# Performance work log

Hardware: AMD Instinct MI355X
Metric: run time of the kernel (lower is better)

Reference implementation:

```python
import jax, jax.numpy as jnp
import numpy as np
from jax import lax

NPOINT = 2048

def setup_inputs() -> dict:
    key = jax.random.key(0)
    B, C, N = 8, 3, 131072
    xyz = jax.random.normal(key, (B, C, N), dtype=jnp.float32)
    return {"xyz": xyz}

def reference(xyz) -> jnp.ndarray:
    # xyz: [B, 3, N] -> points [B, N, 3], as in the torch permute(0,2,1)
    pts = jnp.transpose(xyz, (0, 2, 1)).astype(jnp.float32)  # [B, N, 3]
    B, N, _ = pts.shape
    binds = jnp.arange(B)

    # PointNet++ furthest point sampling: first sampled index is 0,
    # maintain per-point min squared distance to the sampled set,
    # pick argmax each iteration.
    init_dist = jnp.full((B, N), 1e10, dtype=jnp.float32)
    init_idx = jnp.zeros((B,), dtype=jnp.int32)

    def step(carry, _):
        dist, last_idx = carry
        last = pts[binds, last_idx]                     # [B, 3]
        d = jnp.sum((pts - last[:, None, :]) ** 2, -1)  # [B, N]
        dist = jnp.minimum(dist, d)
        nxt = jnp.argmax(dist, axis=-1).astype(jnp.int32)
        return (dist, nxt), last_idx

    _, idxs = lax.scan(step, (init_dist, init_idx), None, length=NPOINT)
    return jnp.transpose(idxs, (1, 0))  # [B, npoint] int32 indices
```

## Files before the change

kernel.cpp:

```cpp
#include <hip/hip_runtime.h>
#include <stdint.h>


#define NB 8
#define NPTS 131072
#define NPOINT 2048
#define KBLK 32
#define BLOCK 512
#define PPT 8
#define NWAVES (BLOCK / 64)
#define PSTRIDE 8

__device__ uint64_t g_part[NB][KBLK * PSTRIDE];

static __device__ __forceinline__ uint64_t ld_rlx(uint64_t* p) {
  return __hip_atomic_load(p, __ATOMIC_RELAXED, __HIP_MEMORY_SCOPE_AGENT);
}
static __device__ __forceinline__ void st_rlx(uint64_t* p, uint64_t v) {
  __hip_atomic_store(p, v, __ATOMIC_RELAXED, __HIP_MEMORY_SCOPE_AGENT);
}

__global__ __launch_bounds__(BLOCK, 1) void fps_kernel(
    const float* __restrict__ xyz, int* __restrict__ out) {
  const int b = blockIdx.x & (NB - 1);
  const int k = blockIdx.x >> 3;
  const int tid = threadIdx.x;
  const int lane = tid & 63;
  const int wid = tid >> 6;

  const float* __restrict__ X = xyz + (size_t)b * 3u * NPTS;
  const float* __restrict__ Y = X + NPTS;
  const float* __restrict__ Z = Y + NPTS;

  const int base = k * (BLOCK * PPT);

  float px[PPT], py[PPT], pz[PPT], dist[PPT];
#pragma unroll
  for (int j = 0; j < PPT; ++j) {
    int i = base + j * BLOCK + tid;
    px[j] = X[i];
    py[j] = Y[i];
    pz[j] = Z[i];
    dist[j] = 1e10f;
  }

  __shared__ uint64_t sh_w[NWAVES];
  __shared__ int sh_idx;

  if (k == 0 && tid == 0) out[b * NPOINT] = 0;

  int cur = 0;

  for (int r = 1; r < NPOINT; ++r) {
    const int lu = __builtin_amdgcn_readfirstlane(cur);
    const float qx = X[lu];
    const float qy = Y[lu];
    const float qz = Z[lu];

    uint64_t pm = 0;
#pragma unroll
    for (int j = 0; j < PPT; ++j) {
      float dx = __fsub_rn(px[j], qx);
      float dy = __fsub_rn(py[j], qy);
      float dz = __fsub_rn(pz[j], qz);
      float d = __fadd_rn(__fadd_rn(__fmul_rn(dx, dx), __fmul_rn(dy, dy)),
                          __fmul_rn(dz, dz));
      float nd = fminf(dist[j], d);
      dist[j] = nd;
      uint32_t idx = (uint32_t)(base + j * BLOCK + tid);
      uint64_t cand = ((uint64_t)__float_as_uint(nd) << 32) |
                      ((uint64_t)(NPTS - 1u - idx) << 12);
      pm = cand > pm ? cand : pm;
    }

#pragma unroll
    for (int off = 32; off; off >>= 1) {
      uint64_t o = (uint64_t)__shfl_xor((unsigned long long)pm, off, 64);
      pm = o > pm ? o : pm;
    }
    if (lane == 0) sh_w[wid] = pm;
    __syncthreads();

    if (tid < 64) {
      uint64_t bm = (lane < NWAVES) ? sh_w[lane] : 0;
#pragma unroll
      for (int off = 4; off; off >>= 1) {
        uint64_t o = (uint64_t)__shfl_xor((unsigned long long)bm, off, 64);
        bm = o > bm ? o : bm;
      }
      if (tid == 0) st_rlx(&g_part[b][k * PSTRIDE], bm | (uint64_t)(uint32_t)r);

      uint64_t w = 0;
      if (lane < KBLK) {
        uint64_t* pp = &g_part[b][lane * PSTRIDE];
        do {
          w = ld_rlx(pp);
        } while ((w & 0xFFFull) != (uint64_t)(uint32_t)r);
      }
#pragma unroll
      for (int off = 16; off; off >>= 1) {
        uint64_t o = (uint64_t)__shfl_xor((unsigned long long)w, off, 64);
        w = o > w ? o : w;
      }
      if (tid == 0) {
        int widx = (int)(NPTS - 1u - (uint32_t)((w >> 12) & 0x1FFFFu));
        if (k == 0) out[b * NPOINT + r] = widx;
        sh_idx = widx;
      }
    }
    __syncthreads();
    cur = sh_idx;
  }
}

extern "C" void kernel_launch(void* const* d_in, const int* in_sizes, int n_in,
                              void* d_out, int out_size, void* d_ws,
                              size_t ws_size, hipStream_t stream) {
  (void)in_sizes; (void)n_in; (void)d_ws; (void)ws_size; (void)out_size;
  const float* xyz = (const float*)d_in[0];
  int* out = (int*)d_out;
  fps_kernel<<<dim3(NB * KBLK), dim3(BLOCK), 0, stream>>>(xyz, out);
}
```

Measured before the change: 4.581 ms.

## Replace block barriers with per-wave global slots and wave-level polling

Drops both __syncthreads per iteration. Each wave now publishes its own tagged partial max to a global slot (256 per batch), and every wave independently polls all slots and reduces them itself. This removes intra-block barrier latency and the single-wave serialization step. In exchange it adds global polling traffic from 8x more waves and denser slots with no padding, which may cause cache-line contention.

Measured after the change: 16.49 ms. 260% more time.

```diff
diff --git a/kernel.cpp b/kernel.cpp
--- a/kernel.cpp
+++ b/kernel.cpp
@@ -8,16 +8,21 @@
 #define KBLK 32
 #define BLOCK 512
 #define PPT 8
-#define NWAVES (BLOCK / 64)
-#define PSTRIDE 8
+#define WPB (BLOCK / 64)
+#define NSLOT (KBLK * WPB)
+#define SPL (NSLOT / 64)
 
-__device__ uint64_t g_part[NB][KBLK * PSTRIDE];
+__device__ uint64_t g_part[NB][NSLOT];
 
 static __device__ __forceinline__ uint64_t ld_rlx(uint64_t* p) {
   return __hip_atomic_load(p, __ATOMIC_RELAXED, __HIP_MEMORY_SCOPE_AGENT);
 }
 static __device__ __forceinline__ void st_rlx(uint64_t* p, uint64_t v) {
   __hip_atomic_store(p, v, __ATOMIC_RELAXED, __HIP_MEMORY_SCOPE_AGENT);
+}
+
+static __device__ __forceinline__ uint64_t max64(uint64_t a, uint64_t b) {
+  return a > b ? a : b;
 }
 
 __global__ __launch_bounds__(BLOCK, 1) void fps_kernel(
@@ -27,6 +32,7 @@
   const int tid = threadIdx.x;
   const int lane = tid & 63;
   const int wid = tid >> 6;
+  const int slot = k * WPB + wid;
 
   const float* __restrict__ X = xyz + (size_t)b * 3u * NPTS;
   const float* __restrict__ Y = X + NPTS;
@@ -43,9 +49,6 @@
     pz[j] = Z[i];
     dist[j] = 1e10f;
   }
-
-  __shared__ uint64_t sh_w[NWAVES];
-  __shared__ int sh_idx;
 
   if (k == 0 && tid == 0) out[b * NPOINT] = 0;
 
@@ -70,46 +73,40 @@
       uint32_t idx = (uint32_t)(base + j * BLOCK + tid);
       uint64_t cand = ((uint64_t)__float_as_uint(nd) << 32) |
                       ((uint64_t)(NPTS - 1u - idx) << 12);
-      pm = cand > pm ? cand : pm;
+      pm = max64(pm, cand);
     }
 
 #pragma unroll
     for (int off = 32; off; off >>= 1) {
       uint64_t o = (uint64_t)__shfl_xor((unsigned long long)pm, off, 64);
-      pm = o > pm ? o : pm;
+      pm = max64(pm, o);
     }
-    if (lane == 0) sh_w[wid] = pm;
-    __syncthreads();
 
-    if (tid < 64) {
-      uint64_t bm = (lane < NWAVES) ? sh_w[lane] : 0;
+    if (lane == 0) st_rlx(&g_part[b][slot], pm | (uint64_t)(uint32_t)r);
+
+    uint64_t* gp = &g_part[b][0];
+    uint64_t w0, w1, w2, w3;
+    const uint32_t tag = (uint32_t)r;
+    for (;;) {
+      w0 = ld_rlx(gp + lane);
+      w1 = ld_rlx(gp + lane + 64);
+      w2 = ld_rlx(gp + lane + 128);
+      w3 = ld_rlx(gp + lane + 192);
+      uint64_t bad = ((w0 ^ tag) | (w1 ^ tag) | (w2 ^ tag) | (w3 ^ tag)) &
+                     0xFFFull;
+      if (bad == 0) break;
+    }
+
+    uint64_t m = max64(max64(w0, w1), max64(w2, w3));
 #pragma unroll
-      for (int off = 4; off; off >>= 1) {
-        uint64_t o = (uint64_t)__shfl_xor((unsigned long long)bm, off, 64);
-        bm = o > bm ? o : bm;
-      }
-      if (tid == 0) st_rlx(&g_part[b][k * PSTRIDE], bm | (uint64_t)(uint32_t)r);
+    for (int off = 32; off; off >>= 1) {
+      uint64_t o = (uint64_t)__shfl_xor((unsigned long long)m, off, 64);
+      m = max64(m, o);
+    }
 
-      uint64_t w = 0;
-      if (lane < KBLK) {
-        uint64_t* pp = &g_part[b][lane * PSTRIDE];
-        do {
-          w = ld_rlx(pp);
-        } while ((w & 0xFFFull) != (uint64_t)(uint32_t)r);
-      }
-#pragma unroll
-      for (int off = 16; off; off >>= 1) {
-        uint64_t o = (uint64_t)__shfl_xor((unsigned long long)w, off, 64);
-        w = o > w ? o : w;
-      }
-      if (tid == 0) {
-        int widx = (int)(NPTS - 1u - (uint32_t)((w >> 12) & 0x1FFFFu));
-        if (k == 0) out[b * NPOINT + r] = widx;
-        sh_idx = widx;
-      }
-    }
-    __syncthreads();
-    cur = sh_idx;
+    int widx = (int)(NPTS - 1u - (uint32_t)((m >> 12) & 0x1FFFFu));
+    if (k == 0 && tid == 0) out[b * NPOINT + r] = widx;
+    cur = widx;
   }
 }
 
```
